# Optimization experiments

Measured on AMD Instinct MI355X. Metric: run time of the kernel, lower is better.

## Reference

```python
import jax, jax.numpy as jnp
import numpy as np

B, S, D, E, R, TOP_K = 4, 4096, 2048, 6, 16, 2


def setup_inputs() -> dict:
    key = jax.random.key(0)
    ks = jax.random.split(key, 9)
    scale = 0.02
    return {
        "x": jax.random.normal(ks[0], (B, S, D), dtype=jnp.float32),
        "W_base": jax.random.normal(ks[1], (D, D), dtype=jnp.float32) * scale,
        "b_base": jax.random.normal(ks[2], (D,), dtype=jnp.float32) * scale,
        "A_s": jax.random.normal(ks[3], (D, R), dtype=jnp.float32) * scale,   # shared expert down-proj
        "B_s": jax.random.normal(ks[4], (R, D), dtype=jnp.float32) * scale,   # shared expert up-proj
        "A_r": jax.random.normal(ks[5], (E, D, R), dtype=jnp.float32) * scale,  # routed experts down-proj
        "B_r": jax.random.normal(ks[6], (E, R, D), dtype=jnp.float32) * scale,  # routed experts up-proj
        "W_router": jax.random.normal(ks[7], (D, E), dtype=jnp.float32) * scale,
        "b_router": jax.random.normal(ks[8], (E,), dtype=jnp.float32) * scale,
    }


def reference(x, W_base, b_base, A_s, B_s, A_r, B_r, W_router, b_router):
    # base_out computed under torch.no_grad() in the original -> stop_gradient
    base_out = jax.lax.stop_gradient(jnp.einsum("bsd,df->bsf", x, W_base) + b_base)

    # single shared LoRA expert (num_shared=1)
    shared_out = jnp.einsum("bsr,rf->bsf", jnp.einsum("bsd,dr->bsr", x, A_s), B_s)

    # router: softmax over experts, then top-k gating
    gates = jax.nn.softmax(jnp.einsum("bsd,de->bse", x, W_router) + b_router, axis=-1)
    topk_w, topk_i = jax.lax.top_k(gates, TOP_K)  # [B,S,K]
    # per-expert combine weight: sum of top-k weights scattered to expert slots
    w_per_e = jnp.sum(topk_w[..., None] * jax.nn.one_hot(topk_i, E, dtype=x.dtype), axis=2)  # [B,S,E]

    # routed LoRA experts: rank-16 down-proj per expert, weight in low-rank space,
    # then up-proj -- avoids materializing the [B,S,E,D] expert outputs.
    h = jnp.einsum("bsd,edr->bser", x, A_r)          # [B,S,E,R]
    hw = h * w_per_e[..., None]                       # fold gate weights into rank dim
    routed_out = jnp.einsum("bser,erf->bsf", hw, B_r)  # [B,S,D]

    return base_out + shared_out + routed_out
```

## Files before the change

kernel.cpp:

```cpp
#include <hip/hip_runtime.h>
#include <hip/hip_bf16.h>

typedef __hip_bfloat16 bf16;
typedef __attribute__((ext_vector_type(8))) __bf16 bf16x8;
typedef __attribute__((ext_vector_type(8))) short s16x8;
typedef __attribute__((ext_vector_type(4))) float f32x4;

#define AS1 __attribute__((address_space(1)))
#define AS3 __attribute__((address_space(3)))

#define DDIM 2048
#define KDIM 2176
#define TTOK 16384


__global__ __launch_bounds__(256) void prep_kernel(
    const float* __restrict__ W, const float* __restrict__ A_s,
    const float* __restrict__ A_r, const float* __restrict__ Bs,
    const float* __restrict__ Br, const float* __restrict__ Wr,
    bf16* __restrict__ Wcat, bf16* __restrict__ AcT, float* __restrict__ WrT) {
  __shared__ bf16 tl[64][65];
  int bid = blockIdx.x, tid = threadIdx.x;
  if (bid < 1024) {
    int bi = bid >> 5, bj = bid & 31;
    int k0 = bi * 64, n0 = bj * 64;
    int r = tid >> 2, c0 = (tid & 3) << 4;
#pragma unroll
    for (int q = 0; q < 4; ++q) {
      f32x4 v = *(const f32x4*)(W + (long)(k0 + r) * DDIM + n0 + c0 + q * 4);
#pragma unroll
      for (int j = 0; j < 4; ++j) tl[r][c0 + q * 4 + j] = __float2bfloat16(v[j]);
    }
    __syncthreads();
    __align__(16) bf16 o[16];
#pragma unroll
    for (int i = 0; i < 16; ++i) o[i] = tl[c0 + i][r];
    *(s16x8*)(Wcat + (long)(n0 + r) * KDIM + k0 + c0) = *(const s16x8*)o;
    *(s16x8*)(Wcat + (long)(n0 + r) * KDIM + k0 + c0 + 8) = *(const s16x8*)(o + 8);
  } else if (bid < 2048) {
    int idx = (bid - 1024) * 256 + tid;
    int c = idx >> 11, d = idx & 2047;
    float v = 0.f;
    if (c < 16)       v = A_s[d * 16 + c];
    else if (c < 112) { int cr = c - 16; v = A_r[((long)(cr >> 4) * DDIM + d) * 16 + (cr & 15)]; }
    AcT[(long)c * DDIM + d] = __float2bfloat16(v);
  } else if (bid < 3072) {
    int idx = (bid - 2048) * 256 + tid;
    int n = idx >> 7, c = idx & 127;
    float v = 0.f;
    if (c < 16)       v = Bs[c * DDIM + n];
    else if (c < 112) v = Br[(long)(c - 16) * DDIM + n];
    Wcat[(long)n * KDIM + 2048 + c] = __float2bfloat16(v);
  } else {
    int idx = (bid - 3072) * 256 + tid;
    int e = idx >> 11, d = idx & 2047;
    WrT[e * 2048 + d] = Wr[d * 6 + e];
  }
}


__global__ __launch_bounds__(256) void conv_router_kernel(
    const float* __restrict__ x, const float* __restrict__ WrT, const float* __restrict__ br,
    bf16* __restrict__ xh, float* __restrict__ gates) {
  int tid = threadIdx.x;
  int d0 = tid * 8;
  long t0 = (long)blockIdx.x * 4;

  f32x4 wa[6], wb[6];
#pragma unroll
  for (int e = 0; e < 6; ++e) {
    wa[e] = *(const f32x4*)(WrT + e * 2048 + d0);
    wb[e] = *(const f32x4*)(WrT + e * 2048 + d0 + 4);
  }

  float p[4][6];
#pragma unroll
  for (int s = 0; s < 4; ++s) {
    long t = t0 + s;
    f32x4 v0 = *(const f32x4*)(x + t * DDIM + d0);
    f32x4 v1 = *(const f32x4*)(x + t * DDIM + d0 + 4);
    __align__(16) bf16 tmp[8];
#pragma unroll
    for (int j = 0; j < 4; ++j) {
      tmp[j] = __float2bfloat16(v0[j]);
      tmp[4 + j] = __float2bfloat16(v1[j]);
    }
    *(s16x8*)(xh + t * KDIM + d0) = *(const s16x8*)tmp;
#pragma unroll
    for (int e = 0; e < 6; ++e) {
      float sum = 0.f;
#pragma unroll
      for (int j = 0; j < 4; ++j) sum += v0[j] * wa[e][j];
#pragma unroll
      for (int j = 0; j < 4; ++j) sum += v1[j] * wb[e][j];
      p[s][e] = sum;
    }
  }

#pragma unroll
  for (int off = 32; off > 0; off >>= 1)
#pragma unroll
    for (int s = 0; s < 4; ++s)
#pragma unroll
      for (int e = 0; e < 6; ++e) p[s][e] += __shfl_down(p[s][e], off);

  __shared__ float red[4][4][6];
  int wave = tid >> 6, lane = tid & 63;
  if (lane == 0)
#pragma unroll
    for (int s = 0; s < 4; ++s)
#pragma unroll
      for (int e = 0; e < 6; ++e) red[s][wave][e] = p[s][e];
  __syncthreads();
  if (tid < 4) {
    int s = tid;
    float g[6], mx = -1e30f;
#pragma unroll
    for (int e = 0; e < 6; ++e) {
      g[e] = red[s][0][e] + red[s][1][e] + red[s][2][e] + red[s][3][e] + br[e];
      mx = fmaxf(mx, g[e]);
    }
    float sm = 0.f;
#pragma unroll
    for (int e = 0; e < 6; ++e) { g[e] = __expf(g[e] - mx); sm += g[e]; }
    float inv = 1.f / sm;
#pragma unroll
    for (int e = 0; e < 6; ++e) g[e] *= inv;
    int i1 = 0; float w1 = g[0];
#pragma unroll
    for (int e = 1; e < 6; ++e) if (g[e] > w1) { w1 = g[e]; i1 = e; }
    int i2 = -1; float w2 = -1.f;
#pragma unroll
    for (int e = 0; e < 6; ++e) if (e != i1 && g[e] > w2) { w2 = g[e]; i2 = e; }
#pragma unroll
    for (int e = 0; e < 6; ++e)
      gates[(t0 + s) * 6 + e] = (e == i1) ? w1 : (e == i2) ? w2 : 0.f;
  }
}


template <int ROWS>
__device__ __forceinline__ void stage_tile(const bf16* __restrict__ g, long rs,
                                           bf16* lds, int wave, int lane) {
#pragma unroll
  for (int i = 0; i < (ROWS >> 5); ++i) {
    int chunk_base = (i * 4 + wave) * 64;
    int byte = (chunk_base + lane) * 16;
    int row = byte >> 7;
    int col = (byte & 127) >> 1;
    __builtin_amdgcn_global_load_lds(
        (const AS1 void*)(g + (long)row * rs + col),
        (AS3 void*)(lds + chunk_base * 8), 16, 0, 0);
  }
}


__global__ __launch_bounds__(256) void lora_kernel(
    bf16* __restrict__ xh, const bf16* __restrict__ AcT,
    const float* __restrict__ gates) {
  __shared__ __align__(16) short smem[2 * 192 * 64];
  __shared__ float G[64][6];
  int tid = threadIdx.x, wave = tid >> 6, lane = tid & 63;
  long m0 = (long)blockIdx.x * 64;

  auto Xbuf = [&](int b) { return (bf16*)smem + b * 192 * 64; };
  auto Bbuf = [&](int b) { return (bf16*)smem + b * 192 * 64 + 64 * 64; };

  stage_tile<64>(xh + m0 * KDIM, KDIM, Xbuf(0), wave, lane);
  stage_tile<128>(AcT, DDIM, Bbuf(0), wave, lane);
  for (int i = tid; i < 384; i += 256) G[i / 6][i % 6] = gates[(m0 + i / 6) * 6 + i % 6];
  __syncthreads();

  f32x4 acc[7];
#pragma unroll
  for (int i = 0; i < 7; ++i) acc[i] = f32x4{0.f, 0.f, 0.f, 0.f};

  for (int kt = 0; kt < 32; ++kt) {
    int cur = kt & 1;
    if (kt < 31) {
      int k1 = (kt + 1) * 64;
      stage_tile<64>(xh + m0 * KDIM + k1, KDIM, Xbuf(cur ^ 1), wave, lane);
      stage_tile<128>(AcT + k1, DDIM, Bbuf(cur ^ 1), wave, lane);
    }
    if (kt > 0) {
      if (kt < 31) asm volatile("s_waitcnt vmcnt(6)" ::: "memory");
      else         asm volatile("s_waitcnt vmcnt(0)" ::: "memory");
      __builtin_amdgcn_sched_barrier(0);
      __builtin_amdgcn_s_barrier();
      __builtin_amdgcn_sched_barrier(0);
    }
    bf16* X_s = Xbuf(cur);
    bf16* B_s = Bbuf(cur);
#pragma unroll
    for (int kk = 0; kk < 2; ++kk) {
      bf16x8 a = *(const bf16x8*)(X_s + (16 * wave + (lane & 15)) * 64 + kk * 32 + (lane >> 4) * 8);
#pragma unroll
      for (int nr = 0; nr < 7; ++nr) {
        bf16x8 b = *(const bf16x8*)(B_s + (16 * nr + (lane & 15)) * 64 + kk * 32 + (lane >> 4) * 8);
        acc[nr] = __builtin_amdgcn_mfma_f32_16x16x32_bf16(a, b, acc[nr], 0, 0, 0);
      }
    }
    __builtin_amdgcn_sched_barrier(0);
    __builtin_amdgcn_s_barrier();
  }

  bf16* H = (bf16*)smem;
#pragma unroll
  for (int nr = 0; nr < 7; ++nr) {
    int c = nr * 16 + (lane & 15);
#pragma unroll
    for (int reg = 0; reg < 4; ++reg) {
      int tl = 16 * wave + 4 * (lane >> 4) + reg;
      float wgt = (c < 16) ? 1.f : G[tl][(c - 16) >> 4];
      H[tl * 128 + c] = __float2bfloat16(acc[nr][reg] * wgt);
    }
  }
  {
    int c = 112 + (lane & 15);
#pragma unroll
    for (int reg = 0; reg < 4; ++reg) {
      int tl = 16 * wave + 4 * (lane >> 4) + reg;
      H[tl * 128 + c] = __float2bfloat16(0.f);
    }
  }
  __syncthreads();
#pragma unroll
  for (int p = 0; p < 4; ++p) {
    int v = p * 256 + tid;
    int row = v >> 4, ch = (v & 15) * 8;
    *(s16x8*)(xh + (m0 + row) * KDIM + 2048 + ch) = *(const s16x8*)(H + row * 128 + ch);
  }
}


__global__ __launch_bounds__(512, 2) void gemm256_kernel(
    const bf16* __restrict__ xh, const bf16* __restrict__ Wcat,
    const float* __restrict__ b_base, float* __restrict__ out) {
  extern __shared__ char sm[];
  int tid = threadIdx.x, wave = tid >> 6, lane = tid & 63;
  int wr = wave >> 2, wc = wave & 3;

  int bid = blockIdx.x;
  int cpx = gridDim.x >> 3;
  int swz = (bid & 7) * cpx + (bid >> 3);
  long m0 = (long)(swz >> 3) * 256;
  int n0 = (swz & 7) * 256;

  int cp = ((lane >> 4) << 4) ^ (((lane >> 1) & 3) << 4);

  float bias[4];
#pragma unroll
  for (int nf = 0; nf < 4; ++nf) bias[nf] = b_base[n0 + wc * 64 + nf * 16 + (lane & 15)];

  f32x4 acc[8][4];
#pragma unroll
  for (int i = 0; i < 8; ++i)
#pragma unroll
    for (int j = 0; j < 4; ++j) acc[i][j] = f32x4{0.f, 0.f, 0.f, 0.f};

  const bf16* Agl = xh + m0 * KDIM;
  const bf16* Bgl = Wcat + (long)n0 * KDIM;

  auto stage_sub = [&](int t, int op, int h, int s) {
    int row = tid >> 2;
    int scol = ((((tid & 3) << 4) ^ (((row >> 1) & 3) << 4)) >> 1);
    const bf16* src = (op ? Bgl : Agl) + (long)(h * 128 + row) * KDIM + t * 64 + s * 32 + scol;
    char* dst = sm + (t & 1) * 65536 + op * 32768 + (h * 2 + s) * 8192 + tid * 16;
    __builtin_amdgcn_global_load_lds((const AS1 void*)src, (AS3 void*)dst, 16, 0, 0);
  };

  bf16x8 a[4], b[4];

  auto phase = [&](int buf, int ks, int mh, bool doStage, int stT, int stOp, int stKs, int vm) {
    if (mh == 0) {
      char* Bb = sm + buf * 65536 + 32768 + ((wc >> 1) * 2 + ks) * 8192;
#pragma unroll
      for (int n = 0; n < 4; ++n)
        b[n] = *(const bf16x8*)(Bb + ((wc & 1) * 64 + n * 16 + (lane & 15)) * 64 + cp);
    }
    char* Ab = sm + buf * 65536 + (wr * 2 + ks) * 8192;
#pragma unroll
    for (int j = 0; j < 4; ++j)
      a[j] = *(const bf16x8*)(Ab + ((mh * 4 + j) * 16 + (lane & 15)) * 64 + cp);
    if (doStage) { stage_sub(stT, stOp, 0, stKs); stage_sub(stT, stOp, 1, stKs); }
    __builtin_amdgcn_s_barrier();
    __builtin_amdgcn_s_setprio(1);
#pragma unroll
    for (int j = 0; j < 4; ++j)
#pragma unroll
      for (int n = 0; n < 4; ++n)
        acc[mh * 4 + j][n] = __builtin_amdgcn_mfma_f32_16x16x32_bf16(a[j], b[n], acc[mh * 4 + j][n], 0, 0, 0);
    __builtin_amdgcn_s_setprio(0);
    if (vm == 6)      asm volatile("s_waitcnt vmcnt(6)" ::: "memory");
    else if (vm == 4) asm volatile("s_waitcnt vmcnt(4)" ::: "memory");
    else if (vm == 0) asm volatile("s_waitcnt vmcnt(0)" ::: "memory");
    __builtin_amdgcn_s_barrier();
  };

  stage_sub(0, 0, 0, 0); stage_sub(0, 0, 1, 0); stage_sub(0, 1, 0, 0); stage_sub(0, 1, 1, 0);
  stage_sub(0, 0, 0, 1); stage_sub(0, 0, 1, 1); stage_sub(0, 1, 0, 1); stage_sub(0, 1, 1, 1);
  stage_sub(1, 0, 0, 0); stage_sub(1, 0, 1, 0); stage_sub(1, 1, 0, 0); stage_sub(1, 1, 1, 0);
  asm volatile("s_waitcnt vmcnt(8)" ::: "memory");
  __builtin_amdgcn_s_barrier();

  for (int i = 0; i < 16; ++i) {
    int t0 = 2 * i;
    phase(0, 0, 0, true, t0 + 1, 0, 1, -1);
    phase(0, 0, 1, true, t0 + 1, 1, 1, 6);
    phase(0, 1, 0, true, t0 + 2, 0, 0, -1);
    phase(0, 1, 1, true, t0 + 2, 1, 0, 6);
    phase(1, 0, 0, true, t0 + 2, 0, 1, -1);
    phase(1, 0, 1, true, t0 + 2, 1, 1, 6);
    phase(1, 1, 0, true, t0 + 3, 0, 0, -1);
    phase(1, 1, 1, true, t0 + 3, 1, 0, 6);
  }
  phase(0, 0, 0, true, 33, 0, 1, -1);
  phase(0, 0, 1, true, 33, 1, 1, 6);
  phase(0, 1, 0, false, 0, 0, 0, -1);
  phase(0, 1, 1, false, 0, 0, 0, 0);
  phase(1, 0, 0, false, 0, 0, 0, -1);
  phase(1, 0, 1, false, 0, 0, 0, -1);
  phase(1, 1, 0, false, 0, 0, 0, -1);
  phase(1, 1, 1, false, 0, 0, 0, -1);

  float* Cs = (float*)sm;
#pragma unroll
  for (int p = 0; p < 2; ++p) {
    __syncthreads();
#pragma unroll
    for (int q = 0; q < 4; ++q) {
#pragma unroll
      for (int nf = 0; nf < 4; ++nf) {
#pragma unroll
        for (int reg = 0; reg < 4; ++reg) {
          int r = wr * 64 + q * 16 + 4 * (lane >> 4) + reg;
          int colb = ((wc * 64 + nf * 16 + (lane & 15)) * 4) ^ (((r >> 2) & 3) << 6);
          *(float*)((char*)Cs + r * 1024 + colb) = acc[p * 4 + q][nf][reg] + bias[nf];
        }
      }
    }
    __syncthreads();
#pragma unroll 4
    for (int it = 0; it < 16; ++it) {
      int v = it * 512 + tid;
      int r = v >> 6, slot = v & 63;
      f32x4 val = *(const f32x4*)((char*)Cs + r * 1024 + ((slot << 4) ^ (((r >> 2) & 3) << 6)));
      long grow = m0 + (r >> 6) * 128 + p * 64 + (r & 63);
      *(f32x4*)(out + grow * DDIM + n0 + slot * 4) = val;
    }
  }
}


extern "C" void kernel_launch(void* const* d_in, const int* in_sizes, int n_in,
                              void* d_out, int out_size, void* d_ws, size_t ws_size,
                              hipStream_t stream) {
  const float* x        = (const float*)d_in[0];
  const float* W_base   = (const float*)d_in[1];
  const float* b_base   = (const float*)d_in[2];
  const float* A_s      = (const float*)d_in[3];
  const float* B_s      = (const float*)d_in[4];
  const float* A_r      = (const float*)d_in[5];
  const float* B_r      = (const float*)d_in[6];
  const float* W_router = (const float*)d_in[7];
  const float* b_router = (const float*)d_in[8];
  float* out = (float*)d_out;

  char* ws = (char*)d_ws;
  bf16*  xh    = (bf16*)(ws);
  bf16*  Wcat  = (bf16*)(ws + 71303168);
  bf16*  AcT   = (bf16*)(ws + 80216064);
  float* gates = (float*)(ws + 80740352);
  float* WrT   = (float*)(ws + 81133568);

  (void)hipFuncSetAttribute((const void*)gemm256_kernel,
                            hipFuncAttributeMaxDynamicSharedMemorySize, 131072);

  prep_kernel<<<3120, 256, 0, stream>>>(W_base, A_s, A_r, B_s, B_r, W_router, Wcat, AcT, WrT);
  conv_router_kernel<<<TTOK / 4, 256, 0, stream>>>(x, WrT, b_router, xh, gates);
  lora_kernel<<<256, 256, 0, stream>>>(xh, AcT, gates);
  gemm256_kernel<<<512, 512, 131072, stream>>>(xh, Wcat, b_base, out);
}
```

Measured before the change: 228.7 us.

## Halve GEMM phase barriers and retile LoRA kernel to 32-row blocks

The main GEMM pipeline drops the barrier between the LDS fragment reads and the MFMAs, and keeps the trailing barrier only on every second phase. This cuts workgroup barrier stalls while relying on the staging and vmcnt ordering to keep double-buffered LDS reuse safe. Separately, the LoRA down-projection kernel now uses 32-token tiles with a 2x2 wave split across the rank columns, so it launches twice as many blocks for better GPU occupancy. The risk is an LDS write-after-read race in the GEMM if a wave runs ahead into a buffer that other waves are still reading.

```diff
diff --git a/kernel.cpp b/kernel.cpp
--- a/kernel.cpp
+++ b/kernel.cpp
@@ -158,32 +158,33 @@
 __global__ __launch_bounds__(256) void lora_kernel(
     bf16* __restrict__ xh, const bf16* __restrict__ AcT,
     const float* __restrict__ gates) {
-  __shared__ __align__(16) short smem[2 * 192 * 64];
-  __shared__ float G[64][6];
+  __shared__ __align__(16) short smem[2 * 160 * 64];
+  __shared__ float G[32][6];
   int tid = threadIdx.x, wave = tid >> 6, lane = tid & 63;
-  long m0 = (long)blockIdx.x * 64;
-
-  auto Xbuf = [&](int b) { return (bf16*)smem + b * 192 * 64; };
-  auto Bbuf = [&](int b) { return (bf16*)smem + b * 192 * 64 + 64 * 64; };
-
-  stage_tile<64>(xh + m0 * KDIM, KDIM, Xbuf(0), wave, lane);
+  int wm = wave >> 1, wn = wave & 1;
+  long m0 = (long)blockIdx.x * 32;
+
+  auto Xbuf = [&](int b) { return (bf16*)smem + b * 160 * 64; };
+  auto Bbuf = [&](int b) { return (bf16*)smem + b * 160 * 64 + 32 * 64; };
+
+  stage_tile<32>(xh + m0 * KDIM, KDIM, Xbuf(0), wave, lane);
   stage_tile<128>(AcT, DDIM, Bbuf(0), wave, lane);
-  for (int i = tid; i < 384; i += 256) G[i / 6][i % 6] = gates[(m0 + i / 6) * 6 + i % 6];
+  for (int i = tid; i < 192; i += 256) G[i / 6][i % 6] = gates[(m0 + i / 6) * 6 + i % 6];
   __syncthreads();
 
-  f32x4 acc[7];
-#pragma unroll
-  for (int i = 0; i < 7; ++i) acc[i] = f32x4{0.f, 0.f, 0.f, 0.f};
+  f32x4 acc[4];
+#pragma unroll
+  for (int i = 0; i < 4; ++i) acc[i] = f32x4{0.f, 0.f, 0.f, 0.f};
 
   for (int kt = 0; kt < 32; ++kt) {
     int cur = kt & 1;
     if (kt < 31) {
       int k1 = (kt + 1) * 64;
-      stage_tile<64>(xh + m0 * KDIM + k1, KDIM, Xbuf(cur ^ 1), wave, lane);
+      stage_tile<32>(xh + m0 * KDIM + k1, KDIM, Xbuf(cur ^ 1), wave, lane);
       stage_tile<128>(AcT + k1, DDIM, Bbuf(cur ^ 1), wave, lane);
     }
     if (kt > 0) {
-      if (kt < 31) asm volatile("s_waitcnt vmcnt(6)" ::: "memory");
+      if (kt < 31) asm volatile("s_waitcnt vmcnt(5)" ::: "memory");
       else         asm volatile("s_waitcnt vmcnt(0)" ::: "memory");
       __builtin_amdgcn_sched_barrier(0);
       __builtin_amdgcn_s_barrier();
@@ -193,10 +194,10 @@
     bf16* B_s = Bbuf(cur);
 #pragma unroll
     for (int kk = 0; kk < 2; ++kk) {
-      bf16x8 a = *(const bf16x8*)(X_s + (16 * wave + (lane & 15)) * 64 + kk * 32 + (lane >> 4) * 8);
-#pragma unroll
-      for (int nr = 0; nr < 7; ++nr) {
-        bf16x8 b = *(const bf16x8*)(B_s + (16 * nr + (lane & 15)) * 64 + kk * 32 + (lane >> 4) * 8);
+      bf16x8 a = *(const bf16x8*)(X_s + (wm * 16 + (lane & 15)) * 64 + kk * 32 + (lane >> 4) * 8);
+#pragma unroll
+      for (int nr = 0; nr < 4; ++nr) {
+        bf16x8 b = *(const bf16x8*)(B_s + (wn * 64 + nr * 16 + (lane & 15)) * 64 + kk * 32 + (lane >> 4) * 8);
         acc[nr] = __builtin_amdgcn_mfma_f32_16x16x32_bf16(a, b, acc[nr], 0, 0, 0);
       }
     }
@@ -206,26 +207,18 @@
 
   bf16* H = (bf16*)smem;
 #pragma unroll
-  for (int nr = 0; nr < 7; ++nr) {
-    int c = nr * 16 + (lane & 15);
+  for (int nr = 0; nr < 4; ++nr) {
+    int c = wn * 64 + nr * 16 + (lane & 15);
 #pragma unroll
     for (int reg = 0; reg < 4; ++reg) {
-      int tl = 16 * wave + 4 * (lane >> 4) + reg;
-      float wgt = (c < 16) ? 1.f : G[tl][(c - 16) >> 4];
+      int tl = wm * 16 + 4 * (lane >> 4) + reg;
+      float wgt = (c < 16) ? 1.f : (c < 112 ? G[tl][(c - 16) >> 4] : 0.f);
       H[tl * 128 + c] = __float2bfloat16(acc[nr][reg] * wgt);
     }
   }
-  {
-    int c = 112 + (lane & 15);
-#pragma unroll
-    for (int reg = 0; reg < 4; ++reg) {
-      int tl = 16 * wave + 4 * (lane >> 4) + reg;
-      H[tl * 128 + c] = __float2bfloat16(0.f);
-    }
-  }
   __syncthreads();
 #pragma unroll
-  for (int p = 0; p < 4; ++p) {
+  for (int p = 0; p < 2; ++p) {
     int v = p * 256 + tid;
     int row = v >> 4, ch = (v & 15) * 8;
     *(s16x8*)(xh + (m0 + row) * KDIM + 2048 + ch) = *(const s16x8*)(H + row * 128 + ch);
@@ -271,7 +264,8 @@
 
   bf16x8 a[4], b[4];
 
-  auto phase = [&](int buf, int ks, int mh, bool doStage, int stT, int stOp, int stKs, int vm) {
+  auto phase = [&](int buf, int ks, int mh, bool doStage, int stT, int stOp, int stKs,
+                   int vm, bool bar) {
     if (mh == 0) {
       char* Bb = sm + buf * 65536 + 32768 + ((wc >> 1) * 2 + ks) * 8192;
 #pragma unroll
@@ -283,7 +277,6 @@
     for (int j = 0; j < 4; ++j)
       a[j] = *(const bf16x8*)(Ab + ((mh * 4 + j) * 16 + (lane & 15)) * 64 + cp);
     if (doStage) { stage_sub(stT, stOp, 0, stKs); stage_sub(stT, stOp, 1, stKs); }
-    __builtin_amdgcn_s_barrier();
     __builtin_amdgcn_s_setprio(1);
 #pragma unroll
     for (int j = 0; j < 4; ++j)
@@ -292,9 +285,8 @@
         acc[mh * 4 + j][n] = __builtin_amdgcn_mfma_f32_16x16x32_bf16(a[j], b[n], acc[mh * 4 + j][n], 0, 0, 0);
     __builtin_amdgcn_s_setprio(0);
     if (vm == 6)      asm volatile("s_waitcnt vmcnt(6)" ::: "memory");
-    else if (vm == 4) asm volatile("s_waitcnt vmcnt(4)" ::: "memory");
     else if (vm == 0) asm volatile("s_waitcnt vmcnt(0)" ::: "memory");
-    __builtin_amdgcn_s_barrier();
+    if (bar) __builtin_amdgcn_s_barrier();
   };
 
   stage_sub(0, 0, 0, 0); stage_sub(0, 0, 1, 0); stage_sub(0, 1, 0, 0); stage_sub(0, 1, 1, 0);
@@ -305,23 +297,23 @@
 
   for (int i = 0; i < 16; ++i) {
     int t0 = 2 * i;
-    phase(0, 0, 0, true, t0 + 1, 0, 1, -1);
-    phase(0, 0, 1, true, t0 + 1, 1, 1, 6);
-    phase(0, 1, 0, true, t0 + 2, 0, 0, -1);
-    phase(0, 1, 1, true, t0 + 2, 1, 0, 6);
-    phase(1, 0, 0, true, t0 + 2, 0, 1, -1);
-    phase(1, 0, 1, true, t0 + 2, 1, 1, 6);
-    phase(1, 1, 0, true, t0 + 3, 0, 0, -1);
-    phase(1, 1, 1, true, t0 + 3, 1, 0, 6);
-  }
-  phase(0, 0, 0, true, 33, 0, 1, -1);
-  phase(0, 0, 1, true, 33, 1, 1, 6);
-  phase(0, 1, 0, false, 0, 0, 0, -1);
-  phase(0, 1, 1, false, 0, 0, 0, 0);
-  phase(1, 0, 0, false, 0, 0, 0, -1);
-  phase(1, 0, 1, false, 0, 0, 0, -1);
-  phase(1, 1, 0, false, 0, 0, 0, -1);
-  phase(1, 1, 1, false, 0, 0, 0, -1);
+    phase(0, 0, 0, true, t0 + 1, 0, 1, -1, false);
+    phase(0, 0, 1, true, t0 + 1, 1, 1, 6, true);
+    phase(0, 1, 0, true, t0 + 2, 0, 0, -1, false);
+    phase(0, 1, 1, true, t0 + 2, 1, 0, 6, true);
+    phase(1, 0, 0, true, t0 + 2, 0, 1, -1, false);
+    phase(1, 0, 1, true, t0 + 2, 1, 1, 6, true);
+    phase(1, 1, 0, true, t0 + 3, 0, 0, -1, false);
+    phase(1, 1, 1, true, t0 + 3, 1, 0, 6, true);
+  }
+  phase(0, 0, 0, true, 33, 0, 1, -1, false);
+  phase(0, 0, 1, true, 33, 1, 1, 6, true);
+  phase(0, 1, 0, false, 0, 0, 0, -1, false);
+  phase(0, 1, 1, false, 0, 0, 0, 0, true);
+  phase(1, 0, 0, false, 0, 0, 0, -1, false);
+  phase(1, 0, 1, false, 0, 0, 0, -1, false);
+  phase(1, 1, 0, false, 0, 0, 0, -1, false);
+  phase(1, 1, 1, false, 0, 0, 0, -1, false);
 
   float* Cs = (float*)sm;
 #pragma unroll
@@ -378,6 +370,6 @@
 
   prep_kernel<<<3120, 256, 0, stream>>>(W_base, A_s, A_r, B_s, B_r, W_router, Wcat, AcT, WrT);
   conv_router_kernel<<<TTOK / 4, 256, 0, stream>>>(x, WrT, b_router, xh, gates);
-  lora_kernel<<<256, 256, 0, stream>>>(xh, AcT, gates);
+  lora_kernel<<<512, 256, 0, stream>>>(xh, AcT, gates);
   gemm256_kernel<<<512, 512, 131072, stream>>>(xh, Wcat, b_base, out);
 }
```

Result: faster. 219.4 us (-4.0%).
